# Kernel optimization log

Measured on AMD Instinct MI355X. Metric: run time of the kernel, lower is better.

Reference implementation:

```python
import jax, jax.numpy as jnp
import numpy as np

B, N, C = 2, 1024, 81          # images, proposals/img, classes (class 0 = background)
H, W = 1024, 1024              # image size
D = 100                        # detections_per_img
WX, WY, WW, WH = 10.0, 10.0, 5.0, 5.0   # BoxCoder weights
SCORE_THRESH = 0.05
NMS_THRESH = 0.5
BBOX_XFORM_CLIP = float(np.log(1000.0 / 16.0))
NEG = -1e30
TO_REMOVE = 1.0


def setup_inputs() -> dict:
    key = jax.random.key(0)
    k1, k2, k3, k4 = jax.random.split(key, 4)
    class_logits = jax.random.normal(k1, (B, N, C), jnp.float32)
    regression_outputs = jax.random.normal(k2, (B, N, C * 4), jnp.float32) * 0.5
    # build valid xyxy proposal boxes inside the image
    cxy = jax.random.uniform(k3, (B, N, 2), jnp.float32, 0.0, W - 1.0)
    wh = jax.random.uniform(k4, (B, N, 2), jnp.float32, 8.0, 256.0)
    x1y1 = jnp.clip(cxy - wh / 2, 0.0, W - 1.0)
    x2y2 = jnp.clip(cxy + wh / 2, 0.0, W - 1.0)
    proposals = jnp.concatenate([x1y1, x2y2], axis=-1)
    return dict(class_logits=class_logits,
                regression_outputs=regression_outputs,
                proposals=proposals)


def decode(rel, props):
    # rel: [N, C, 4], props: [N, 4] xyxy -> decoded per-class boxes [N, C, 4], clipped to image
    widths = props[:, 2] - props[:, 0] + TO_REMOVE   # [N]
    heights = props[:, 3] - props[:, 1] + TO_REMOVE
    ctr_x = props[:, 0] + 0.5 * widths
    ctr_y = props[:, 1] + 0.5 * heights
    dx = rel[..., 0] / WX
    dy = rel[..., 1] / WY
    dw = jnp.minimum(rel[..., 2] / WW, BBOX_XFORM_CLIP)
    dh = jnp.minimum(rel[..., 3] / WH, BBOX_XFORM_CLIP)
    pcx = dx * widths[:, None] + ctr_x[:, None]
    pcy = dy * heights[:, None] + ctr_y[:, None]
    pw = jnp.exp(dw) * widths[:, None]
    ph = jnp.exp(dh) * heights[:, None]
    x1 = pcx - 0.5 * pw
    y1 = pcy - 0.5 * ph
    x2 = pcx + 0.5 * pw - 1.0
    y2 = pcy + 0.5 * ph - 1.0
    # clip_to_image
    x1 = jnp.clip(x1, 0.0, W - TO_REMOVE)
    y1 = jnp.clip(y1, 0.0, H - TO_REMOVE)
    x2 = jnp.clip(x2, 0.0, W - TO_REMOVE)
    y2 = jnp.clip(y2, 0.0, H - TO_REMOVE)
    return jnp.stack([x1, y1, x2, y2], axis=-1)


def pairwise_iou(b):
    # b: [N, 4] -> [N, N]
    area = (b[:, 2] - b[:, 0] + TO_REMOVE) * (b[:, 3] - b[:, 1] + TO_REMOVE)
    lt = jnp.maximum(b[:, None, :2], b[None, :, :2])
    rb = jnp.minimum(b[:, None, 2:], b[None, :, 2:])
    wh = jnp.clip(rb - lt + TO_REMOVE, 0.0)
    inter = wh[..., 0] * wh[..., 1]
    return inter / (area[:, None] + area[None, :] - inter)


def nms_keep(boxes, scores):
    # boxes [N,4], scores [N] (NEG for below-threshold boxes) -> keep mask [N] bool
    order = jnp.argsort(-scores)
    b = boxes[order]
    iou = pairwise_iou(b)                       # [N, N]
    valid = scores[order] > NEG / 2             # below-threshold boxes never participate
    idx = jnp.arange(N)

    def body(i, keep):
        sup = keep[i] & (iou[i] > NMS_THRESH) & (idx > i)
        return keep & ~sup

    keep_sorted = jax.lax.fori_loop(0, N, body, valid)
    return jnp.zeros(N, bool).at[order].set(keep_sorted)


def _per_image(logits, rel, props):
    probs = jax.nn.softmax(logits, axis=-1)                 # [N, C]
    boxes = decode(rel.reshape(N, C, 4), props)             # [N, C, 4]
    cls_boxes = jnp.transpose(boxes[:, 1:, :], (1, 0, 2))   # [C-1, N, 4]  (skip background)
    cls_scores = probs[:, 1:].T                              # [C-1, N]
    valid = cls_scores > SCORE_THRESH
    masked_in = jnp.where(valid, cls_scores, NEG)
    keep = jax.vmap(nms_keep)(cls_boxes, masked_in)          # [C-1, N]
    surv = jnp.where(keep & valid, cls_scores, NEG)
    top_scores, top_idx = jax.lax.top_k(surv.reshape(-1), D)  # over (C-1)*N candidates
    cls_idx = top_idx // N
    box_idx = top_idx % N
    sel_boxes = cls_boxes[cls_idx, box_idx]                  # [D, 4]
    labels = cls_idx + 1
    ok = top_scores > NEG / 2
    return (jnp.where(ok[:, None], sel_boxes, 0.0),
            jnp.where(ok, top_scores, 0.0),
            jnp.where(ok, labels, -1))


def reference(class_logits, regression_outputs, proposals):
    # returns (boxes [B,D,4], scores [B,D], labels [B,D]); invalid slots zeroed / label -1
    return jax.vmap(_per_image)(class_logits, regression_outputs, proposals)
```

## Files before the change

### kernel.cpp

```cpp
#include <hip/hip_runtime.h>
#include <math.h>
#include <float.h>

#define BN 2
#define NP 1024
#define NC 81
#define NCLS 80
#define ND 100
#define NSLOT 64
#define CAP2 512
#define CAPT 512
#define NBIN 4096
#define SCORE_T 0.05f
#define NMS_T 0.5f
#define BBOX_CLIP 4.135166556742356f

typedef unsigned long long ull;

__device__ __forceinline__ void decode_box(
    const float* __restrict__ props, const float* __restrict__ regress,
    int b, int n, int c, float& x1, float& y1, float& x2, float& y2)
{
    const float* pr = props + ((size_t)b * NP + n) * 4;
    float p0 = pr[0], p1 = pr[1], p2 = pr[2], p3 = pr[3];
    float w  = p2 - p0 + 1.0f, h = p3 - p1 + 1.0f;
    float cx = p0 + 0.5f * w,  cy = p1 + 0.5f * h;
    const float* rl = regress + (((size_t)b * NP + n) * NC + c) * 4;
    float dx = rl[0] / 10.0f, dy = rl[1] / 10.0f;
    float dw = fminf(rl[2] / 5.0f, BBOX_CLIP);
    float dh = fminf(rl[3] / 5.0f, BBOX_CLIP);
    float pcx = dx * w + cx, pcy = dy * h + cy;
    float pw  = expf(dw) * w, ph = expf(dh) * h;
    x1 = pcx - 0.5f * pw; y1 = pcy - 0.5f * ph;
    x2 = pcx + 0.5f * pw - 1.0f; y2 = pcy + 0.5f * ph - 1.0f;
    x1 = fminf(fmaxf(x1, 0.f), 1023.f);
    y1 = fminf(fmaxf(y1, 0.f), 1023.f);
    x2 = fminf(fmaxf(x2, 0.f), 1023.f);
    y2 = fminf(fmaxf(y2, 0.f), 1023.f);
}

__device__ __forceinline__ void emit_slot(
    float* __restrict__ out, const float* __restrict__ props,
    const float* __restrict__ regress, int b, int d, ull key)
{
    float score = __uint_as_float((unsigned int)(key >> 32));
    float* ob = out + ((size_t)b * ND + d) * 4;
    float* os = out + (size_t)BN * ND * 4 + b * ND + d;
    float* ol = out + (size_t)BN * ND * 5 + b * ND + d;
    if (score > 0.f) {
        unsigned int f = 0xFFFFFFFFu - (unsigned int)(key & 0xFFFFFFFFu);
        int cls = f / NP, n = f % NP;
        float x1, y1, x2, y2;
        decode_box(props, regress, b, n, cls + 1, x1, y1, x2, y2);
        ob[0] = x1; ob[1] = y1; ob[2] = x2; ob[3] = y2;
        *os = score;
        *ol = (float)(cls + 1);
    } else {
        ob[0] = 0.f; ob[1] = 0.f; ob[2] = 0.f; ob[3] = 0.f;
        *os = 0.f;
        *ol = -1.f;
    }
}

__device__ __forceinline__ void bitonic_desc(ull* a, int len, int tid, int nthr)
{
    for (int k = 2; k <= len; k <<= 1) {
        for (int j = k >> 1; j > 0; j >>= 1) {
            for (int i = tid; i < len; i += nthr) {
                int ixj = i ^ j;
                if (ixj > i) {
                    bool desc = ((i & k) == 0);
                    ull x = a[i], y = a[ixj];
                    if (desc ? (x < y) : (x > y)) { a[i] = y; a[ixj] = x; }
                }
            }
            __syncthreads();
        }
    }
}

__global__ __launch_bounds__(256) void nms_kernel(
    const float* __restrict__ logits, const float* __restrict__ regress,
    const float* __restrict__ props, ull* __restrict__ g_key)
{
    const int tid  = threadIdx.x;
    const int l    = tid & 63;
    const int wave = tid >> 6;
    const int idx  = blockIdx.x;
    const int b    = idx / NCLS;
    const int cls  = idx % NCLS;
    const int c    = cls + 1;

    __shared__ struct {
        ull   key[CAP2];
        float x1[CAP2], y1[CAP2], x2[CAP2], y2[CAP2], area[CAP2];
        int   keep[CAP2];
    } sm;
    __shared__ int s_cnt, s_app;

    if (tid == 0) { s_cnt = 0; s_app = 0; }
    __syncthreads();

    #pragma unroll 1
    for (int k = 0; k < 4; ++k) {
        int r = tid + k * 256;
        const float* row = logits + ((size_t)b * NP + r) * NC;
        float v[NC];
        #pragma unroll
        for (int i = 0; i < NC; ++i) v[i] = row[i];
        float m = -FLT_MAX;
        #pragma unroll
        for (int i = 0; i < NC; ++i) m = fmaxf(m, v[i]);
        float s = 0.f;
        #pragma unroll
        for (int i = 0; i < NC; ++i) s += expf(v[i] - m);
        float lc = row[c];
        float p = expf(lc - m) / s;
        if (p > SCORE_T) {
            int kk = atomicAdd(&s_cnt, 1);
            if (kk < CAP2)
                sm.key[kk] = ((ull)__float_as_uint(p) << 32)
                           | (ull)(0xFFFFFFFFu - (unsigned)r);
        }
    }
    __syncthreads();
    int M = s_cnt; if (M > CAP2) M = CAP2;
    ull* g_slot = g_key + (size_t)idx * NSLOT;

    if (M > 64) {
        int Mp = 128; while (Mp < M) Mp <<= 1;
        for (int i = M + tid; i < Mp; i += 256) sm.key[i] = 0ull;
        __syncthreads();
        bitonic_desc(sm.key, Mp, tid, 256);
        for (int i = tid; i < M; i += 256) {
            int n = (int)(0xFFFFFFFFu - (unsigned)(sm.key[i] & 0xFFFFFFFFu));
            float x1, y1, x2, y2;
            decode_box(props, regress, b, n, c, x1, y1, x2, y2);
            sm.x1[i] = x1; sm.y1[i] = y1; sm.x2[i] = x2; sm.y2[i] = y2;
            sm.area[i] = (x2 - x1 + 1.f) * (y2 - y1 + 1.f);
            sm.keep[i] = 1;
        }
        __syncthreads();
        for (int i = 0; i < M; ++i) {
            if (sm.keep[i]) {
                float x1i = sm.x1[i], y1i = sm.y1[i];
                float x2i = sm.x2[i], y2i = sm.y2[i], ai = sm.area[i];
                for (int j = i + 1 + tid; j < M; j += 256) {
                    float lx = fmaxf(x1i, sm.x1[j]);
                    float ly = fmaxf(y1i, sm.y1[j]);
                    float rx = fminf(x2i, sm.x2[j]);
                    float ry = fminf(y2i, sm.y2[j]);
                    float wd = fmaxf(rx - lx + 1.f, 0.f);
                    float ht = fmaxf(ry - ly + 1.f, 0.f);
                    float inter = wd * ht;
                    float iou = inter / (ai + sm.area[j] - inter);
                    if (iou > NMS_T) sm.keep[j] = 0;
                }
            }
            __syncthreads();
        }
        for (int i = tid; i < M; i += 256) {
            if (sm.keep[i]) {
                int pos = atomicAdd(&s_app, 1);
                if (pos < NSLOT) {
                    ull key = sm.key[i];
                    unsigned n = 0xFFFFFFFFu - (unsigned)(key & 0xFFFFFFFFu);
                    unsigned f = (unsigned)cls * NP + n;
                    g_slot[pos] = (key & 0xFFFFFFFF00000000ull)
                                | (ull)(0xFFFFFFFFu - f);
                }
            }
        }
        __syncthreads();
        int st = s_app; if (st > NSLOT) st = NSLOT;
        for (int i = st + tid; i < NSLOT; i += 256) g_slot[i] = 0ull;
    } else {
        if (wave == 0) {
            ull key = (l < M) ? sm.key[l] : 0ull;
            #pragma unroll
            for (int k = 2; k <= 64; k <<= 1) {
                #pragma unroll
                for (int j = k >> 1; j > 0; j >>= 1) {
                    ull p = __shfl_xor(key, j, 64);
                    bool lower = (l & j) == 0;
                    bool up    = (l & k) != 0;
                    ull mn = key < p ? key : p;
                    ull mx = key < p ? p : key;
                    key = (lower == up) ? mn : mx;
                }
            }
            float x1 = 0.f, y1 = 0.f, x2 = 0.f, y2 = 0.f, ar = 0.f;
            if (l < M) {
                int n = (int)(0xFFFFFFFFu - (unsigned)(key & 0xFFFFFFFFu));
                decode_box(props, regress, b, n, c, x1, y1, x2, y2);
                ar = (x2 - x1 + 1.f) * (y2 - y1 + 1.f);
            }
            ull keep = (M >= 64) ? ~0ull : ((1ull << M) - 1ull);
            for (int i = 0; i < M; ++i) {
                if ((keep >> i) & 1ull) {
                    float xi1 = __shfl(x1, i, 64), yi1 = __shfl(y1, i, 64);
                    float xi2 = __shfl(x2, i, 64), yi2 = __shfl(y2, i, 64);
                    float ari = __shfl(ar, i, 64);
                    float lx = fmaxf(xi1, x1), ly = fmaxf(yi1, y1);
                    float rx = fminf(xi2, x2), ry = fminf(yi2, y2);
                    float wd = fmaxf(rx - lx + 1.f, 0.f);
                    float ht = fmaxf(ry - ly + 1.f, 0.f);
                    float inter = wd * ht;
                    float iou = inter / (ari + ar - inter);
                    ull sup = __ballot(iou > NMS_T && l > i);
                    keep &= ~sup;
                }
            }
            ull vout = 0ull;
            if ((keep >> l) & 1ull) {
                unsigned n = 0xFFFFFFFFu - (unsigned)(key & 0xFFFFFFFFu);
                unsigned f = (unsigned)cls * NP + n;
                vout = (key & 0xFFFFFFFF00000000ull) | (ull)(0xFFFFFFFFu - f);
            }
            g_slot[l] = vout;
        }
    }
}

__global__ __launch_bounds__(256) void topk_kernel(
    ull* __restrict__ g_key, const float* __restrict__ props,
    const float* __restrict__ regress, float* __restrict__ out)
{
    const int b   = blockIdx.x;
    const int tid = threadIdx.x;
    const int l   = tid & 63;
    const int wave = tid >> 6;

    __shared__ int hist[NBIN];
    __shared__ ull cbuf[CAPT];
    __shared__ ull rk[256];
    __shared__ int rp[256];
    __shared__ int s_bstar, s_cnt2;

    const int K = NCLS * NSLOT;
    ull* keys = g_key + (size_t)b * K;

    for (int i = tid; i < NBIN; i += 256) hist[i] = 0;
    if (tid == 0) s_cnt2 = 0;
    __syncthreads();
    for (int i = tid; i < K; i += 256) {
        ull key = keys[i];
        if (key) atomicAdd(&hist[(int)(key >> 52)], 1);
    }
    __syncthreads();

    if (tid < 64) {
        int gs = 0;
        for (int q = 0; q < 64; ++q) gs += hist[l * 64 + q];
        int pre = gs;
        for (int off = 1; off < 64; off <<= 1) {
            int vv = __shfl_up(pre, off, 64);
            if (l >= off) pre += vv;
        }
        int total = __shfl(pre, 63, 64);
        int S = total - pre + gs;
        ull ball = __ballot(S >= ND);
        int gstar = ball ? (63 - __clzll((long long)ball)) : 0;
        int Sg = __shfl(S, gstar, 64);
        int Gg = __shfl(gs, gstar, 64);
        int A  = Sg - Gg;
        int h  = hist[gstar * 64 + l];
        int pre2 = h;
        for (int off = 1; off < 64; off <<= 1) {
            int vv = __shfl_up(pre2, off, 64);
            if (l >= off) pre2 += vv;
        }
        int T = Gg - pre2 + h;
        ull ball2 = __ballot(A + T >= ND);
        int binin = ball2 ? (63 - __clzll((long long)ball2)) : 0;
        if (l == 0) s_bstar = gstar * 64 + binin;
    }
    __syncthreads();
    const int bstar = s_bstar;

    for (int i = tid; i < K; i += 256) {
        ull key = keys[i];
        if (key && (int)(key >> 52) >= bstar) {
            int p = atomicAdd(&s_cnt2, 1);
            if (p < CAPT) cbuf[p] = key;
        }
    }
    __syncthreads();
    const int Tt = s_cnt2;

    if (Tt <= 256) {
        if (wave == 0) {
            ull key4[4];
            #pragma unroll
            for (int r = 0; r < 4; ++r) {
                int e = r * 64 + l;
                key4[r] = (e < Tt) ? cbuf[e] : 0ull;
            }
            #pragma unroll
            for (int k = 2; k <= 256; k <<= 1) {
                #pragma unroll
                for (int j = k >> 1; j > 0; j >>= 1) {
                    if (j >= 64) {
                        int d = j >> 6;
                        #pragma unroll
                        for (int r = 0; r < 4; ++r) {
                            if ((r & d) == 0) {
                                int e = r * 64 + l;
                                bool desc = ((e & k) == 0);
                                ull aa = key4[r], bb = key4[r | d];
                                if (desc ? (aa < bb) : (aa > bb)) {
                                    key4[r] = bb; key4[r | d] = aa;
                                }
                            }
                        }
                    } else {
                        #pragma unroll
                        for (int r = 0; r < 4; ++r) {
                            ull p = __shfl_xor(key4[r], j, 64);
                            int e = r * 64 + l;
                            bool desc = ((e & k) == 0);
                            bool low  = ((l & j) == 0);
                            ull mn = key4[r] < p ? key4[r] : p;
                            ull mx = key4[r] < p ? p : key4[r];
                            key4[r] = (low == desc) ? mx : mn;
                        }
                    }
                }
            }
            emit_slot(out, props, regress, b, l, key4[0]);
            if (l < ND - 64) emit_slot(out, props, regress, b, 64 + l, key4[1]);
        }
    } else if (Tt <= CAPT) {
        int Tp = 512;
        for (int i = Tt + tid; i < Tp; i += 256) cbuf[i] = 0ull;
        __syncthreads();
        bitonic_desc(cbuf, Tp, tid, 256);
        for (int d = tid; d < ND; d += 256)
            emit_slot(out, props, regress, b, d, cbuf[d]);
    } else {
        for (int d = 0; d < ND; ++d) {
            ull bk = 0ull; int bp = -1;
            for (int t = tid; t < K; t += 256) {
                ull k2 = keys[t];
                if (k2 > bk) { bk = k2; bp = t; }
            }
            rk[tid] = bk; rp[tid] = bp;
            __syncthreads();
            for (int off = 128; off > 0; off >>= 1) {
                if (tid < off && rk[tid + off] > rk[tid]) {
                    rk[tid] = rk[tid + off]; rp[tid] = rp[tid + off];
                }
                __syncthreads();
            }
            if (tid == 0) {
                emit_slot(out, props, regress, b, d, rk[0]);
                if (rp[0] >= 0) keys[rp[0]] = 0ull;
            }
            __syncthreads();
        }
    }
}

extern "C" void kernel_launch(void* const* d_in, const int* in_sizes, int n_in,
                              void* d_out, int out_size, void* d_ws, size_t ws_size,
                              hipStream_t stream) {
    const float* logits  = (const float*)d_in[0];
    const float* regress = (const float*)d_in[1];
    const float* props   = (const float*)d_in[2];
    float* out = (float*)d_out;

    ull* g_key = (ull*)d_ws;

    hipLaunchKernelGGL(nms_kernel, dim3(BN * NCLS), dim3(256), 0, stream,
                       logits, regress, props, g_key);
    hipLaunchKernelGGL(topk_kernel, dim3(BN), dim3(256), 0, stream,
                       g_key, props, regress, out);
}
```

Baseline: 98.86 us.

## Precompute softmax row max and sum once in a separate stats kernel

Adds a small kernel that computes each proposal row's logit max and exp-sum once and stores them in workspace. The NMS kernel then reads one logit plus the two stats per row instead of recomputing the full 81-wide softmax reduction in each of the 80 per-class blocks. This removes 80x redundant logit reads and exp work, at the cost of an extra kernel launch and a serial 81-element loop per thread in the stats kernel with strided, uncoalesced row reads.

Measured after the change: 99.51 us. Within noise of the previous version (+0.7%).

```diff
diff --git a/kernel.cpp b/kernel.cpp
--- a/kernel.cpp
+++ b/kernel.cpp
@@ -79,9 +79,23 @@
     }
 }
 
+__global__ __launch_bounds__(64) void stats_kernel(
+    const float* __restrict__ logits, float* __restrict__ mx, float* __restrict__ se)
+{
+    int g = blockIdx.x * 64 + threadIdx.x;
+    const float* row = logits + (size_t)g * NC;
+    float m = -FLT_MAX;
+    for (int i = 0; i < NC; ++i) m = fmaxf(m, row[i]);
+    float s = 0.f;
+    for (int i = 0; i < NC; ++i) s += expf(row[i] - m);
+    mx[g] = m;
+    se[g] = s;
+}
+
 __global__ __launch_bounds__(256) void nms_kernel(
     const float* __restrict__ logits, const float* __restrict__ regress,
-    const float* __restrict__ props, ull* __restrict__ g_key)
+    const float* __restrict__ props, const float* __restrict__ mx,
+    const float* __restrict__ se, ull* __restrict__ g_key)
 {
     const int tid  = threadIdx.x;
     const int l    = tid & 63;
@@ -101,21 +115,11 @@
     if (tid == 0) { s_cnt = 0; s_app = 0; }
     __syncthreads();
 
-    #pragma unroll 1
+    #pragma unroll
     for (int k = 0; k < 4; ++k) {
         int r = tid + k * 256;
-        const float* row = logits + ((size_t)b * NP + r) * NC;
-        float v[NC];
-        #pragma unroll
-        for (int i = 0; i < NC; ++i) v[i] = row[i];
-        float m = -FLT_MAX;
-        #pragma unroll
-        for (int i = 0; i < NC; ++i) m = fmaxf(m, v[i]);
-        float s = 0.f;
-        #pragma unroll
-        for (int i = 0; i < NC; ++i) s += expf(v[i] - m);
-        float lc = row[c];
-        float p = expf(lc - m) / s;
+        int g = b * NP + r;
+        float p = expf(logits[(size_t)g * NC + c] - mx[g]) / se[g];
         if (p > SCORE_T) {
             int kk = atomicAdd(&s_cnt, 1);
             if (kk < CAP2)
@@ -185,8 +189,8 @@
                     bool lower = (l & j) == 0;
                     bool up    = (l & k) != 0;
                     ull mn = key < p ? key : p;
-                    ull mx = key < p ? p : key;
-                    key = (lower == up) ? mn : mx;
+                    ull mx2 = key < p ? p : key;
+                    key = (lower == up) ? mn : mx2;
                 }
             }
             float x1 = 0.f, y1 = 0.f, x2 = 0.f, y2 = 0.f, ar = 0.f;
@@ -321,8 +325,8 @@
                             bool desc = ((e & k) == 0);
                             bool low  = ((l & j) == 0);
                             ull mn = key4[r] < p ? key4[r] : p;
-                            ull mx = key4[r] < p ? p : key4[r];
-                            key4[r] = (low == desc) ? mx : mn;
+                            ull mx2 = key4[r] < p ? p : key4[r];
+                            key4[r] = (low == desc) ? mx2 : mn;
                         }
                     }
                 }
@@ -369,10 +373,15 @@
     const float* props   = (const float*)d_in[2];
     float* out = (float*)d_out;
 
-    ull* g_key = (ull*)d_ws;
-
+    char* ws = (char*)d_ws;
+    float* mx    = (float*)(ws);
+    float* se    = (float*)(ws + 8192);
+    ull*   g_key = (ull*)  (ws + 16384);
+
+    hipLaunchKernelGGL(stats_kernel, dim3(BN * NP / 64), dim3(64), 0, stream,
+                       logits, mx, se);
     hipLaunchKernelGGL(nms_kernel, dim3(BN * NCLS), dim3(256), 0, stream,
-                       logits, regress, props, g_key);
+                       logits, regress, props, mx, se, g_key);
     hipLaunchKernelGGL(topk_kernel, dim3(BN), dim3(256), 0, stream,
                        g_key, props, regress, out);
 }
```
